# Kernel tuning notes

Measured on AMD Instinct MI355X. Metric: run time of the kernel, lower is better.

The kernel has to match this reference:

```python
import jax, jax.numpy as jnp
import numpy as np


def setup_inputs() -> dict:
    key = jax.random.key(0)
    k1, k2, k3 = jax.random.split(key, 3)
    B, IN, OUT, K = 4096, 4096, 2048, 32
    x = jax.random.normal(k1, (B, IN), dtype=jnp.float32)
    values = jax.random.normal(k2, (OUT * K,), dtype=jnp.float32)
    cols = jax.random.randint(k3, (OUT, K), 0, IN, dtype=jnp.int32)
    return {"x": x, "values": values, "cols": cols}


def reference(x, values, cols):
    # out[b, o] = sum_j values[o*K + j] * x[b, cols[o, j]]
    # (equivalent to torch.sparse.mm(w_sparse, x.T).T with fixed K nnz per row)
    OUT, K = cols.shape
    vals = values.reshape(OUT, K)          # [O, K]
    xg = x[:, cols]                        # gather -> [B, O, K]
    return jnp.einsum('bok,ok->bo', xg, vals)  # [B, O]
```

## Files before the change

kernel.cpp:

```cpp
#include <hip/hip_runtime.h>

#define Bdim   4096
#define INdim  4096
#define OUTdim 2048
#define Knz    32

__device__ inline unsigned short f2bf(float f) {
  unsigned u = __float_as_uint(f);
  u += 0x7fffu + ((u >> 16) & 1u);
  return (unsigned short)(u >> 16);
}

__global__ __launch_bounds__(256) void k_transpose(const float* __restrict__ x,
                                                   unsigned short* __restrict__ xT) {
  __shared__ float tile[64][65];
  const int bi = blockIdx.x;
  const int ii = blockIdx.y;
  const int t = threadIdx.x;
  const int r = t >> 4;
  const int c = t & 15;
#pragma unroll
  for (int rr = 0; rr < 64; rr += 16) {
    const float4 v = *reinterpret_cast<const float4*>(
        &x[(size_t)(bi * 64 + rr + r) * INdim + ii * 64 + c * 4]);
    tile[rr + r][c * 4 + 0] = v.x;
    tile[rr + r][c * 4 + 1] = v.y;
    tile[rr + r][c * 4 + 2] = v.z;
    tile[rr + r][c * 4 + 3] = v.w;
  }
  __syncthreads();
#pragma unroll
  for (int rr = 0; rr < 64; rr += 16) {
    const int il = rr + r;
    ushort4 o;
    o.x = f2bf(tile[c * 4 + 0][il]);
    o.y = f2bf(tile[c * 4 + 1][il]);
    o.z = f2bf(tile[c * 4 + 2][il]);
    o.w = f2bf(tile[c * 4 + 3][il]);
    *reinterpret_cast<ushort4*>(
        &xT[(size_t)(ii * 64 + il) * Bdim + bi * 64 + c * 4]) = o;
  }
}

__global__ __launch_bounds__(256) void k_gather(const unsigned short* __restrict__ xT,
                                                const int* __restrict__ cols,
                                                const float* __restrict__ values,
                                                float* __restrict__ out) {
  const int wg = blockIdx.x;
  const int bb = wg & 7;
  const int ob = wg >> 3;
  const int t = threadIdx.x;
  const int b0 = bb * 512 + t * 2;
  const int obase = ob * 8;

  float acc0[8], acc1[8];
#pragma unroll
  for (int oc = 0; oc < 8; ++oc) {
    const int o = obase + oc;
    const int* __restrict__ cp = cols + o * Knz;
    const float* __restrict__ vp = values + o * Knz;
    float a0 = 0.f, a1 = 0.f;
#pragma unroll
    for (int k = 0; k < Knz; ++k) {
      const int col = cp[k];
      const float val = vp[k];
      const unsigned u = *reinterpret_cast<const unsigned*>(
          &xT[(size_t)col * Bdim + b0]);
      const float x0 = __uint_as_float(u << 16);
      const float x1 = __uint_as_float(u & 0xffff0000u);
      a0 = fmaf(x0, val, a0);
      a1 = fmaf(x1, val, a1);
    }
    acc0[oc] = a0;
    acc1[oc] = a1;
  }
  float4* p0 = reinterpret_cast<float4*>(&out[(size_t)b0 * OUTdim + obase]);
  float4* p1 = reinterpret_cast<float4*>(&out[(size_t)(b0 + 1) * OUTdim + obase]);
  p0[0] = make_float4(acc0[0], acc0[1], acc0[2], acc0[3]);
  p0[1] = make_float4(acc0[4], acc0[5], acc0[6], acc0[7]);
  p1[0] = make_float4(acc1[0], acc1[1], acc1[2], acc1[3]);
  p1[1] = make_float4(acc1[4], acc1[5], acc1[6], acc1[7]);
}

__global__ __launch_bounds__(256) void k_naive(const float* __restrict__ x,
                                               const float* __restrict__ values,
                                               const int* __restrict__ cols,
                                               float* __restrict__ out) {
  const size_t id = (size_t)blockIdx.x * 256 + threadIdx.x;
  const int o = (int)(id % OUTdim);
  const int b = (int)(id / OUTdim);
  float a = 0.f;
  for (int k = 0; k < Knz; ++k) {
    const int col = cols[o * Knz + k];
    a = fmaf(x[(size_t)b * INdim + col], values[o * Knz + k], a);
  }
  out[id] = a;
}

extern "C" void kernel_launch(void* const* d_in, const int* in_sizes, int n_in,
                              void* d_out, int out_size, void* d_ws, size_t ws_size,
                              hipStream_t stream) {
  const float* x = (const float*)d_in[0];
  const float* values = (const float*)d_in[1];
  const int* cols = (const int*)d_in[2];
  float* out = (float*)d_out;

  const size_t need = (size_t)INdim * Bdim * sizeof(unsigned short);
  if (ws_size >= need) {
    unsigned short* xT = (unsigned short*)d_ws;
    k_transpose<<<dim3(64, 64), 256, 0, stream>>>(x, xT);
    k_gather<<<2048, 256, 0, stream>>>(xT, cols, values, out);
  } else {
    k_naive<<<(Bdim * (size_t)OUTdim) / 256, 256, 0, stream>>>(x, values, cols, out);
  }
}
```

Baseline: 73.14 us.

## Retile sparse gather: 4 batch rows per lane, XCD-aware block mapping

The gather kernel now has each lane load 4 consecutive bf16 batch values (uint2) per column index instead of 2. Each wavefront handles 4 output rows, and a workgroup covers 256 batch by 16 outputs. Block indices are remapped so the 8 XCDs each own distinct batch ranges, which should improve L2 locality of xT rows. Occupancy is hinted through launch_bounds(256,4). Wider loads cut the number of gather instructions, at the cost of more accumulator registers and a different write pattern (float4 per batch row).

```diff
diff --git a/kernel.cpp b/kernel.cpp
--- a/kernel.cpp
+++ b/kernel.cpp
@@ -42,44 +42,49 @@
   }
 }
 
-__global__ __launch_bounds__(256) void k_gather(const unsigned short* __restrict__ xT,
-                                                const int* __restrict__ cols,
-                                                const float* __restrict__ values,
-                                                float* __restrict__ out) {
+__global__ __launch_bounds__(256, 4) void k_gather(const unsigned short* __restrict__ xT,
+                                                   const int* __restrict__ cols,
+                                                   const float* __restrict__ values,
+                                                   float* __restrict__ out) {
   const int wg = blockIdx.x;
-  const int bb = wg & 7;
-  const int ob = wg >> 3;
-  const int t = threadIdx.x;
-  const int b0 = bb * 512 + t * 2;
-  const int obase = ob * 8;
+  const int xcd = wg & 7;
+  const int g = wg >> 3;
+  const int bb = xcd + 8 * (g >> 7);
+  const int obg = g & 127;
+  const int w = threadIdx.x >> 6;
+  const int l = threadIdx.x & 63;
+  const int b0 = bb * 256 + l * 4;
+  const int o0 = obg * 16 + w * 4;
 
-  float acc0[8], acc1[8];
+  float acc[4][4];
 #pragma unroll
-  for (int oc = 0; oc < 8; ++oc) {
-    const int o = obase + oc;
+  for (int i = 0; i < 4; ++i)
+#pragma unroll
+    for (int j = 0; j < 4; ++j) acc[i][j] = 0.f;
+
+#pragma unroll
+  for (int oc = 0; oc < 4; ++oc) {
+    const int o = o0 + oc;
     const int* __restrict__ cp = cols + o * Knz;
     const float* __restrict__ vp = values + o * Knz;
-    float a0 = 0.f, a1 = 0.f;
 #pragma unroll
     for (int k = 0; k < Knz; ++k) {
       const int col = cp[k];
       const float val = vp[k];
-      const unsigned u = *reinterpret_cast<const unsigned*>(
+      const uint2 u = *reinterpret_cast<const uint2*>(
           &xT[(size_t)col * Bdim + b0]);
-      const float x0 = __uint_as_float(u << 16);
-      const float x1 = __uint_as_float(u & 0xffff0000u);
-      a0 = fmaf(x0, val, a0);
-      a1 = fmaf(x1, val, a1);
+      acc[oc][0] = fmaf(__uint_as_float(u.x << 16), val, acc[oc][0]);
+      acc[oc][1] = fmaf(__uint_as_float(u.x & 0xffff0000u), val, acc[oc][1]);
+      acc[oc][2] = fmaf(__uint_as_float(u.y << 16), val, acc[oc][2]);
+      acc[oc][3] = fmaf(__uint_as_float(u.y & 0xffff0000u), val, acc[oc][3]);
     }
-    acc0[oc] = a0;
-    acc1[oc] = a1;
   }
-  float4* p0 = reinterpret_cast<float4*>(&out[(size_t)b0 * OUTdim + obase]);
-  float4* p1 = reinterpret_cast<float4*>(&out[(size_t)(b0 + 1) * OUTdim + obase]);
-  p0[0] = make_float4(acc0[0], acc0[1], acc0[2], acc0[3]);
-  p0[1] = make_float4(acc0[4], acc0[5], acc0[6], acc0[7]);
-  p1[0] = make_float4(acc1[0], acc1[1], acc1[2], acc1[3]);
-  p1[1] = make_float4(acc1[4], acc1[5], acc1[6], acc1[7]);
+
+#pragma unroll
+  for (int r = 0; r < 4; ++r) {
+    *reinterpret_cast<float4*>(&out[(size_t)(b0 + r) * OUTdim + o0]) =
+        make_float4(acc[0][r], acc[1][r], acc[2][r], acc[3][r]);
+  }
 }
 
 __global__ __launch_bounds__(256) void k_naive(const float* __restrict__ x,
```

New measurement: 230.5 us. 3.15x slower.
